# Optimization experiments

Hardware: AMD Instinct MI355X
Metric: run time of the kernel (lower is better)

## Reference

```python
import jax, jax.numpy as jnp
import numpy as np

H = 8  # num attention heads

def _ln(x, g, b, eps=1e-5):
    m = jnp.mean(x, -1, keepdims=True)
    v = jnp.mean((x - m) ** 2, -1, keepdims=True)
    return (x - m) / jnp.sqrt(v + eps) * g + b

def _mha(x, Wqkv, bqkv, Wo, bo, bias=None):
    Bn, N, D = x.shape
    d = D // H
    q = (x @ Wqkv[0].T + bqkv[0]).reshape(Bn, N, H, d)
    k = (x @ Wqkv[1].T + bqkv[1]).reshape(Bn, N, H, d)
    v = (x @ Wqkv[2].T + bqkv[2]).reshape(Bn, N, H, d)
    s = jnp.einsum('bihd,bjhd->bhij', q, k) * (1.0 / np.sqrt(d))
    if bias is not None:
        s = s + jnp.transpose(bias, (0, 3, 1, 2))  # [Bn,H,N,N] additive bias
    a = jax.nn.softmax(s, axis=-1)
    o = jnp.einsum('bhij,bjhd->bihd', a, v).reshape(Bn, N, D)
    return o @ Wo.T + bo

def _ffn(x, W1, b1, W2, b2):
    return jax.nn.relu(x @ W1.T + b1) @ W2.T + b2

def _pe(T, dim):
    pos = jnp.arange(T, dtype=jnp.float32)[:, None]
    div = jnp.exp(jnp.arange(0, dim, 2, dtype=jnp.float32) * (-np.log(10000.0) / dim))
    pe = jnp.zeros((T, dim), jnp.float32)
    pe = pe.at[:, 0::2].set(jnp.sin(pos * div))
    pe = pe.at[:, 1::2].set(jnp.cos(pos * div))
    return pe

def reference(pose, W_pose, W_emb, prelu_a, W_bias, gWqkv, gbqkv, gWo, gbo, gln1g, gln1b, gW1, gb1, gW2, gb2, gln2g, gln2b, deW, deb, tWqkv, tbqkv, tWo, tbo, tln1g, tln1b, tW1, tb1, tW2, tb2, tln2g, tln2b, W_out):
    B, C, T, V = pose.shape
    D = W_pose.shape[0]
    p = jnp.transpose(pose, (0, 2, 3, 1))  # [B,T,V,C]
    y = jnp.einsum('btvc,dc->btvd', p, W_pose).reshape(B * T, V, D)
    bias_pre = p[:, :, None, :, :] - p[:, :, :, None, :]  # [B,T,V,V,C] pairwise diffs
    pe = _pe(T, D)
    for i in range(2):
        h = jnp.einsum('btijc,hc->btijh', bias_pre, W_emb[i])  # [B,T,V,V,256]
        h = jnp.where(h >= 0, h, prelu_a[i] * h)               # PReLU
        bias = (jnp.einsum('btijh,gh->btijg', h, W_bias[i]) * (1.0 / np.sqrt(float(H)))).reshape(B * T, V, V, H)
        # GraphEncoder: post-LN transformer block with additive per-head attn bias
        a = _mha(y, gWqkv[i], gbqkv[i], gWo[i], gbo[i], bias)
        y1 = _ln(y + a, gln1g[i], gln1b[i])
        g = _ln(y1 + _ffn(y1, gW1[i], gb1[i], gW2[i], gb2[i]), gln2g[i], gln2b[i])
        g = g @ deW[i].T + deb[i]                              # gat_de linear
        # torch .view(B*V, T, -1): raw memory reinterpretation -> jnp.reshape
        y = g.reshape(B * V, T, D) + pe[None]                  # positional encoding
        mem = y
        # temporal Encoder: post-LN transformer block, no bias
        a = _mha(y, tWqkv[i], tbqkv[i], tWo[i], tbo[i])
        y1 = _ln(y + a, tln1g[i], tln1b[i])
        y = _ln(y1 + _ffn(y1, tW1[i], tb1[i], tW2[i], tb2[i]), tln2g[i], tln2b[i])
        y = (y + mem).reshape(B * T, V, D)
    out = jnp.einsum('bvd,od->bvo', y, W_out)
    out = jnp.where(out >= 0, out, 0.01 * out)  # LeakyReLU
    return out.reshape(B, -1, T, V)

def setup_inputs() -> dict:
    key = jax.random.key(0)
    ks = iter(jax.random.split(key, 64))
    def g(shape, scale):
        return jax.random.normal(next(ks), shape, jnp.float32) * scale
    B, C, T, V = 16, 32, 62, 19
    D, Hd, O = 128, 256, 64
    inp = {
        'pose': g((B, C, T, V), 1.0),
        'W_pose': g((D, C), 1.0 / np.sqrt(C)),
        'W_emb': g((2, Hd, C), 1.0 / np.sqrt(C)),
        'prelu_a': jnp.full((2,), 0.25, jnp.float32),
        'W_bias': g((2, H, Hd), 1.0 / np.sqrt(Hd)),
        'gWqkv': g((2, 3, D, D), 1.0 / np.sqrt(D)),
        'gbqkv': jnp.zeros((2, 3, D), jnp.float32),
        'gWo': g((2, D, D), 1.0 / np.sqrt(D)),
        'gbo': jnp.zeros((2, D), jnp.float32),
        'gln1g': jnp.ones((2, D), jnp.float32), 'gln1b': jnp.zeros((2, D), jnp.float32),
        'gW1': g((2, Hd, D), 1.0 / np.sqrt(D)), 'gb1': jnp.zeros((2, Hd), jnp.float32),
        'gW2': g((2, D, Hd), 1.0 / np.sqrt(Hd)), 'gb2': jnp.zeros((2, D), jnp.float32),
        'gln2g': jnp.ones((2, D), jnp.float32), 'gln2b': jnp.zeros((2, D), jnp.float32),
        'deW': g((2, D, D), 1.0 / np.sqrt(D)), 'deb': jnp.zeros((2, D), jnp.float32),
        'tWqkv': g((2, 3, D, D), 1.0 / np.sqrt(D)),
        'tbqkv': jnp.zeros((2, 3, D), jnp.float32),
        'tWo': g((2, D, D), 1.0 / np.sqrt(D)),
        'tbo': jnp.zeros((2, D), jnp.float32),
        'tln1g': jnp.ones((2, D), jnp.float32), 'tln1b': jnp.zeros((2, D), jnp.float32),
        'tW1': g((2, Hd, D), 1.0 / np.sqrt(D)), 'tb1': jnp.zeros((2, Hd), jnp.float32),
        'tW2': g((2, D, Hd), 1.0 / np.sqrt(Hd)), 'tb2': jnp.zeros((2, D), jnp.float32),
        'tln2g': jnp.ones((2, D), jnp.float32), 'tln2b': jnp.zeros((2, D), jnp.float32),
        'W_out': g((O, D), 1.0 / np.sqrt(D)),
    }
    return inp
```

## Files before the change

### kernel.cpp

```cpp
#include <hip/hip_runtime.h>
#include <hip/hip_bf16.h>
#include <math.h>

#define B_  16
#define C_  32
#define T_  62
#define V_  19
#define D_  128
#define HD_ 256
#define H_  8
#define DH_ 16
#define ROWS 18848
#define BT_ 992
#define BV_ 304

typedef __attribute__((ext_vector_type(8))) short short8v;
typedef __attribute__((ext_vector_type(4))) float f32x4;
typedef __attribute__((ext_vector_type(16))) float f32x16;

struct alignas(8) bf4 { __hip_bfloat16 x, y, z, w; };

__device__ __forceinline__ float bf2f(short s) {
    return __uint_as_float(((unsigned)(unsigned short)s) << 16);
}

__global__ void transpose_kernel(const float* __restrict__ pose, __hip_bfloat16* __restrict__ p_bf) {
    int idx = blockIdx.x * 256 + threadIdx.x;
    if (idx >= B_ * T_ * V_ * C_) return;
    int c = idx & 31;
    int rest = idx >> 5;
    int v = rest % V_;
    int rest2 = rest / V_;
    int t = rest2 % T_;
    int b = rest2 / T_;
    p_bf[idx] = __float2bfloat16(pose[((size_t)((b * C_ + c) * T_ + t)) * V_ + v]);
}

__global__ void wconv_kernel(
        const float* s0, const float* s1, const float* s2, const float* s3,
        const float* s4, const float* s5, const float* s6, const float* s7,
        const float* s8, const float* s9, const float* s10, const float* s11,
        __hip_bfloat16* __restrict__ dst) {
    int idx = blockIdx.x * 256 + threadIdx.x;
    if (idx >= 585728) return;
    const float* s; int base;
    if      (idx <   4096) { s = s0;  base = 0;      }
    else if (idx <  20480) { s = s1;  base = 4096;   }
    else if (idx < 118784) { s = s2;  base = 20480;  }
    else if (idx < 151552) { s = s3;  base = 118784; }
    else if (idx < 217088) { s = s4;  base = 151552; }
    else if (idx < 282624) { s = s5;  base = 217088; }
    else if (idx < 315392) { s = s6;  base = 282624; }
    else if (idx < 413696) { s = s7;  base = 315392; }
    else if (idx < 446464) { s = s8;  base = 413696; }
    else if (idx < 512000) { s = s9;  base = 446464; }
    else if (idx < 577536) { s = s10; base = 512000; }
    else                   { s = s11; base = 577536; }
    dst[idx] = __float2bfloat16(s[idx - base]);
}

__global__ __launch_bounds__(512) void w2_kernel(
        const float* __restrict__ Wbias, const float* __restrict__ Wemb,
        float* __restrict__ w2) {
    int tid = threadIdx.x;
    int layer = tid >> 8, g = (tid >> 5) & 7, c = tid & 31;
    float acc = 0.f;
    for (int hh = 0; hh < HD_; ++hh)
        acc += Wbias[layer * 2048 + g * HD_ + hh] * Wemb[layer * 8192 + hh * C_ + c];
    w2[layer * 256 + g * C_ + c] = acc;
}

template<int N, int K, int EPI, bool HASBIAS, bool O32, bool O16>
__global__ __launch_bounds__(256) void mfma_linear(
        const __hip_bfloat16* __restrict__ A, const __hip_bfloat16* __restrict__ W,
        const float* __restrict__ bias, float* __restrict__ out32,
        __hip_bfloat16* __restrict__ out16) {
    int wave = threadIdx.x >> 6;
    int lane = threadIdx.x & 63;
    int nt = blockIdx.y * 4 + wave;
    int n0 = nt * 32;
    if (n0 >= N) return;
    int r0 = blockIdx.x * 64;
    int r1 = r0 + 32;
    bool has2 = (r1 < ROWS);
    int rl = lane & 31;
    int kk = (lane >> 5) * 8;
    const short* Ab0 = (const short*)A + (size_t)(r0 + rl) * K + kk;
    const short* Ab1 = (const short*)A + (size_t)(r1 + rl) * K + kk;
    const short* Wb  = (const short*)W + (size_t)(n0 + rl) * K + kk;
    f32x16 acc0 = {0.f,0.f,0.f,0.f,0.f,0.f,0.f,0.f,0.f,0.f,0.f,0.f,0.f,0.f,0.f,0.f};
    f32x16 acc1 = acc0;
    #pragma unroll
    for (int kb = 0; kb < K / 16; ++kb) {
        short8v b  = *reinterpret_cast<const short8v*>(Wb  + kb * 16);
        short8v a0 = *reinterpret_cast<const short8v*>(Ab0 + kb * 16);
        acc0 = __builtin_amdgcn_mfma_f32_32x32x16_bf16(a0, b, acc0, 0, 0, 0);
        if (has2) {
            short8v a1 = *reinterpret_cast<const short8v*>(Ab1 + kb * 16);
            acc1 = __builtin_amdgcn_mfma_f32_32x32x16_bf16(a1, b, acc1, 0, 0, 0);
        }
    }
    int oc = n0 + rl;
    float bv = HASBIAS ? bias[oc] : 0.f;
    float freq = 0.f;
    if (EPI == 3) freq = expf(-(float)(oc & ~1) * (9.210340371976184f / 128.f));
    #pragma unroll
    for (int t2 = 0; t2 < 2; ++t2) {
        if (t2 == 1 && !has2) break;
        int rb = t2 ? r1 : r0;
        f32x16 acc = t2 ? acc1 : acc0;
        #pragma unroll
        for (int reg = 0; reg < 16; ++reg) {
            int orow = rb + (reg & 3) + 8 * (reg >> 2) + 4 * (lane >> 5);
            float v = acc[reg] + bv;
            if (EPI == 1) v = fmaxf(v, 0.f);
            if (EPI == 2) v = v >= 0.f ? v : 0.01f * v;
            if (EPI == 3) {
                int t = orow % T_;
                float ang = (float)t * freq;
                v += (oc & 1) ? cosf(ang) : sinf(ang);
            }
            if (O32) out32[(size_t)orow * N + oc] = v;
            if (O16) out16[(size_t)orow * N + oc] = __float2bfloat16(v);
        }
    }
}

__global__ __launch_bounds__(256) void bias2_kernel(
        const __hip_bfloat16* __restrict__ p_bf, const __hip_bfloat16* __restrict__ wemb_bf,
        const float* __restrict__ prelu_a, const float* __restrict__ Wbias,
        const float* __restrict__ w2, float* __restrict__ bias) {
    int bt = blockIdx.x;
    __shared__ float es[V_ * 257];
    __shared__ float ps[V_ * 33];
    __shared__ float f_lds[V_ * 8];
    int tid = threadIdx.x;
    if (tid < V_ * 8) {
        int v = tid >> 3, c4 = (tid & 7) * 4;
        bf4 pv = *reinterpret_cast<const bf4*>(&p_bf[((size_t)(bt * V_ + v)) * C_ + c4]);
        float* d = &ps[v * 33 + c4];
        d[0] = __bfloat162float(pv.x); d[1] = __bfloat162float(pv.y);
        d[2] = __bfloat162float(pv.z); d[3] = __bfloat162float(pv.w);
    }
    __syncthreads();
    {
        float wr[C_];
        const __hip_bfloat16* wrow = wemb_bf + (size_t)tid * C_;
        #pragma unroll
        for (int c4 = 0; c4 < 8; ++c4) {
            bf4 wv = *reinterpret_cast<const bf4*>(wrow + c4 * 4);
            wr[c4 * 4 + 0] = __bfloat162float(wv.x);
            wr[c4 * 4 + 1] = __bfloat162float(wv.y);
            wr[c4 * 4 + 2] = __bfloat162float(wv.z);
            wr[c4 * 4 + 3] = __bfloat162float(wv.w);
        }
        for (int v = 0; v < V_; ++v) {
            const float* pr = &ps[v * 33];
            float acc = 0.f;
            #pragma unroll
            for (int c = 0; c < C_; ++c) acc += pr[c] * wr[c];
            es[v * 257 + tid] = acc;
        }
    }
    if (tid < V_ * 8) {
        int v = tid >> 3, g = tid & 7;
        const float* pr = &ps[v * 33];
        const float* wr = &w2[g * C_];
        float acc = 0.f;
        #pragma unroll
        for (int c = 0; c < C_; ++c) acc += pr[c] * wr[c];
        f_lds[v * 8 + g] = acc;
    }
    __syncthreads();
    if (tid < 190) {
        int i = 0, rem = tid, cnt = V_;
        while (rem >= cnt) { rem -= cnt; ++i; --cnt; }
        int j = i + rem;
        const float a = prelu_a[0];
        const float scale = 0.35355339059327373f;
        const float cL = 0.5f * (1.f + a) * scale;
        const float cA = 0.5f * (1.f - a) * scale;
        const float* ei = es + i * 257;
        const float* ej = es + j * 257;
        float S[H_] = {0.f, 0.f, 0.f, 0.f, 0.f, 0.f, 0.f, 0.f};
        #pragma unroll 4
        for (int hh = 0; hh < HD_; ++hh) {
            float d = ej[hh] - ei[hh];
            float ad = fabsf(d);
            const float* w = Wbias + hh;
            #pragma unroll
            for (int g = 0; g < H_; ++g) S[g] += w[g * HD_] * ad;
        }
        float* bij = bias + ((size_t)bt * (V_ * V_) + i * V_ + j) * H_;
        float* bji = bias + ((size_t)bt * (V_ * V_) + j * V_ + i) * H_;
        #pragma unroll
        for (int g = 0; g < H_; ++g) {
            float lin = cL * (f_lds[j * 8 + g] - f_lds[i * 8 + g]);
            float sym = cA * S[g];
            bij[g] = lin + sym;
            bji[g] = sym - lin;
        }
    }
}

__global__ __launch_bounds__(384) void attn_graph_kernel(
        const __hip_bfloat16* __restrict__ qkv, const float* __restrict__ bias,
        __hip_bfloat16* __restrict__ out) {
    int bt = blockIdx.x;
    int h = blockIdx.y;
    __shared__ float q_lds[V_][20];
    __shared__ float k_lds[V_][20];
    __shared__ float v_lds[V_][20];
    __shared__ float sm[V_][20];
    int tid = threadIdx.x;
    for (int idx = tid; idx < V_ * 2 * 3; idx += 384) {
        int mat = idx / (V_ * 2);
        int rem = idx - mat * (V_ * 2);
        int row = rem >> 1, half = rem & 1;
        short8v v = *reinterpret_cast<const short8v*>(
            qkv + ((size_t)(bt * V_ + row)) * 384 + mat * 128 + h * DH_ + half * 8);
        float* dst = (mat == 0 ? q_lds[row] : (mat == 1 ? k_lds[row] : v_lds[row])) + half * 8;
        #pragma unroll
        for (int u = 0; u < 8; ++u) dst[u] = bf2f(v[u]);
    }
    __syncthreads();
    if (tid < V_ * V_) {
        int i = tid / V_, j = tid - i * V_;
        float acc = 0.f;
        #pragma unroll
        for (int c = 0; c < 4; ++c) {
            float4 qv = *reinterpret_cast<const float4*>(&q_lds[i][4 * c]);
            float4 kv = *reinterpret_cast<const float4*>(&k_lds[j][4 * c]);
            acc += qv.x * kv.x + qv.y * kv.y + qv.z * kv.z + qv.w * kv.w;
        }
        sm[i][j] = acc * 0.25f + bias[((size_t)(bt * V_ + i) * V_ + j) * H_ + h];
    }
    __syncthreads();
    if (tid < V_) {
        float m = -1e30f;
        for (int j = 0; j < V_; ++j) m = fmaxf(m, sm[tid][j]);
        float sum = 0.f;
        for (int j = 0; j < V_; ++j) { float e = __expf(sm[tid][j] - m); sm[tid][j] = e; sum += e; }
        float inv = 1.f / sum;
        for (int j = 0; j < V_; ++j) sm[tid][j] *= inv;
    }
    __syncthreads();
    if (tid < V_ * DH_) {
        int i = tid / DH_, d = tid - i * DH_;
        float o = 0.f;
        #pragma unroll 4
        for (int j = 0; j < V_; ++j) o += sm[i][j] * v_lds[j][d];
        out[((size_t)(bt * V_ + i)) * D_ + h * DH_ + d] = __float2bfloat16(o);
    }
}

__global__ __launch_bounds__(256) void attn_temporal_kernel(
        const __hip_bfloat16* __restrict__ qkv, __hip_bfloat16* __restrict__ out) {
    int b = blockIdx.x;
    int h = blockIdx.y;
    __shared__ float q_lds[T_][20];
    __shared__ float k_lds[T_][20];
    __shared__ float v_lds[T_][20];
    __shared__ float sm[T_][68];
    int tid = threadIdx.x;
    for (int idx = tid; idx < T_ * 2 * 3; idx += 256) {
        int mat = idx / (T_ * 2);
        int rem = idx - mat * (T_ * 2);
        int row = rem >> 1, half = rem & 1;
        short8v v = *reinterpret_cast<const short8v*>(
            qkv + ((size_t)(b * T_ + row)) * 384 + mat * 128 + h * DH_ + half * 8);
        float* dst = (mat == 0 ? q_lds[row] : (mat == 1 ? k_lds[row] : v_lds[row])) + half * 8;
        #pragma unroll
        for (int u = 0; u < 8; ++u) dst[u] = bf2f(v[u]);
    }
    __syncthreads();
    if (tid < T_ * 4) {
        int i = tid >> 2, jt = tid & 3;
        float qreg[16];
        #pragma unroll
        for (int c = 0; c < 4; ++c) {
            float4 qv = *reinterpret_cast<const float4*>(&q_lds[i][4 * c]);
            qreg[4 * c + 0] = qv.x * 0.25f;
            qreg[4 * c + 1] = qv.y * 0.25f;
            qreg[4 * c + 2] = qv.z * 0.25f;
            qreg[4 * c + 3] = qv.w * 0.25f;
        }
        float s[16];
        #pragma unroll
        for (int jj = 0; jj < 16; ++jj) {
            int j = jj * 4 + jt;
            float acc = -1e30f;
            if (j < T_) {
                acc = 0.f;
                const float* kr = k_lds[j];
                #pragma unroll
                for (int c = 0; c < 4; ++c) {
                    float4 kv = *reinterpret_cast<const float4*>(&kr[4 * c]);
                    acc += qreg[4*c+0] * kv.x + qreg[4*c+1] * kv.y
                         + qreg[4*c+2] * kv.z + qreg[4*c+3] * kv.w;
                }
            }
            s[jj] = acc;
        }
        float m = -1e30f;
        #pragma unroll
        for (int jj = 0; jj < 16; ++jj) m = fmaxf(m, s[jj]);
        m = fmaxf(m, __shfl_xor(m, 1, 64));
        m = fmaxf(m, __shfl_xor(m, 2, 64));
        float sum = 0.f;
        #pragma unroll
        for (int jj = 0; jj < 16; ++jj) {
            int j = jj * 4 + jt;
            float e = (j < T_) ? __expf(s[jj] - m) : 0.f;
            s[jj] = e;
            sum += e;
        }
        sum += __shfl_xor(sum, 1, 64);
        sum += __shfl_xor(sum, 2, 64);
        float inv = 1.f / sum;
        #pragma unroll
        for (int jj = 0; jj < 16; ++jj) {
            int j = jj * 4 + jt;
            if (j < T_) sm[i][j] = s[jj] * inv;
        }
    }
    __syncthreads();
    if (tid < T_ * 4) {
        int i = tid >> 2, dg = tid & 3;
        float4 o = {0.f, 0.f, 0.f, 0.f};
        for (int j = 0; j < T_; ++j) {
            float pp = sm[i][j];
            const float4 vv = *reinterpret_cast<const float4*>(&v_lds[j][4 * dg]);
            o.x += pp * vv.x; o.y += pp * vv.y; o.z += pp * vv.z; o.w += pp * vv.w;
        }
        bf4 ov = { __float2bfloat16(o.x), __float2bfloat16(o.y),
                   __float2bfloat16(o.z), __float2bfloat16(o.w) };
        *reinterpret_cast<bf4*>(out + ((size_t)(b * T_ + i)) * D_ + h * DH_ + 4 * dg) = ov;
    }
}

template<bool O32, bool O16>
__global__ __launch_bounds__(64) void ln_add_kernel(
        const float* __restrict__ x, const float* __restrict__ r,
        const float* __restrict__ g, const float* __restrict__ b,
        float* __restrict__ o32, __hip_bfloat16* __restrict__ o16) {
    int row = blockIdx.x;
    int lane = threadIdx.x;
    const float* xr = x + (size_t)row * D_;
    const float* rr = r + (size_t)row * D_;
    float v0 = xr[lane] + rr[lane];
    float v1 = xr[lane + 64] + rr[lane + 64];
    float s = v0 + v1, sq = v0 * v0 + v1 * v1;
    #pragma unroll
    for (int off = 32; off > 0; off >>= 1) {
        s += __shfl_xor(s, off, 64);
        sq += __shfl_xor(sq, off, 64);
    }
    float mean = s * (1.f / 128.f);
    float var = sq * (1.f / 128.f) - mean * mean;
    float rstd = rsqrtf(var + 1e-5f);
    float a0 = (v0 - mean) * rstd * g[lane]      + b[lane];
    float a1 = (v1 - mean) * rstd * g[lane + 64] + b[lane + 64];
    if (O32) {
        float* o = o32 + (size_t)row * D_;
        o[lane] = a0; o[lane + 64] = a1;
    }
    if (O16) {
        __hip_bfloat16* o = o16 + (size_t)row * D_;
        o[lane] = __float2bfloat16(a0); o[lane + 64] = __float2bfloat16(a1);
    }
}

__global__ __launch_bounds__(64) void ln_add_add_kernel(
        const float* __restrict__ x, const float* __restrict__ r,
        const float* __restrict__ g, const float* __restrict__ b,
        float* __restrict__ y, __hip_bfloat16* __restrict__ y_bf) {
    int row = blockIdx.x;
    int lane = threadIdx.x;
    const float* xr = x + (size_t)row * D_;
    const float* rr = r + (size_t)row * D_;
    float v0 = xr[lane] + rr[lane];
    float v1 = xr[lane + 64] + rr[lane + 64];
    float s = v0 + v1, sq = v0 * v0 + v1 * v1;
    #pragma unroll
    for (int off = 32; off > 0; off >>= 1) {
        s += __shfl_xor(s, off, 64);
        sq += __shfl_xor(sq, off, 64);
    }
    float mean = s * (1.f / 128.f);
    float var = sq * (1.f / 128.f) - mean * mean;
    float rstd = rsqrtf(var + 1e-5f);
    float a0 = (v0 - mean) * rstd * g[lane]      + b[lane];
    float a1 = (v1 - mean) * rstd * g[lane + 64] + b[lane + 64];
    float* yp = y + (size_t)row * D_;
    __hip_bfloat16* yb = y_bf + (size_t)row * D_;
    float y0 = yp[lane] + a0;
    float y1v = yp[lane + 64] + a1;
    yp[lane] = y0;       yb[lane] = __float2bfloat16(y0);
    yp[lane + 64] = y1v; yb[lane + 64] = __float2bfloat16(y1v);
}

extern "C" void kernel_launch(void* const* d_in, const int* in_sizes, int n_in,
                              void* d_out, int out_size, void* d_ws, size_t ws_size,
                              hipStream_t stream) {
    const float* pose    = (const float*)d_in[0];
    const float* W_pose  = (const float*)d_in[1];
    const float* W_emb   = (const float*)d_in[2];
    const float* prelu_a = (const float*)d_in[3];
    const float* W_bias  = (const float*)d_in[4];
    const float* gWqkv   = (const float*)d_in[5];
    const float* gbqkv   = (const float*)d_in[6];
    const float* gWo     = (const float*)d_in[7];
    const float* gbo     = (const float*)d_in[8];
    const float* gln1g   = (const float*)d_in[9];
    const float* gln1b   = (const float*)d_in[10];
    const float* gW1     = (const float*)d_in[11];
    const float* gb1     = (const float*)d_in[12];
    const float* gW2     = (const float*)d_in[13];
    const float* gb2     = (const float*)d_in[14];
    const float* gln2g   = (const float*)d_in[15];
    const float* gln2b   = (const float*)d_in[16];
    const float* deW     = (const float*)d_in[17];
    const float* deb     = (const float*)d_in[18];
    const float* tWqkv   = (const float*)d_in[19];
    const float* tbqkv   = (const float*)d_in[20];
    const float* tWo     = (const float*)d_in[21];
    const float* tbo     = (const float*)d_in[22];
    const float* tln1g   = (const float*)d_in[23];
    const float* tln1b   = (const float*)d_in[24];
    const float* tW1     = (const float*)d_in[25];
    const float* tb1     = (const float*)d_in[26];
    const float* tW2     = (const float*)d_in[27];
    const float* tb2     = (const float*)d_in[28];
    const float* tln2g   = (const float*)d_in[29];
    const float* tln2b   = (const float*)d_in[30];
    const float* W_out   = (const float*)d_in[31];

    float* ws = (float*)d_ws;
    __hip_bfloat16* p_bf   = (__hip_bfloat16*)(ws + 0);
    float*          y      = ws + 301568;
    __hip_bfloat16* y_bf   = (__hip_bfloat16*)(ws + 2714112);
    float*          biasbuf= ws + 3920384;
    float*          big    = ws + 6785280;
    __hip_bfloat16* qkv_bf = (__hip_bfloat16*)big;
    float*          tmp    = big;
    __hip_bfloat16* hid_bf = (__hip_bfloat16*)(big + 2412544);
    float*          y1     = big + 4825088;
    __hip_bfloat16* attn_bf= (__hip_bfloat16*)(ws + 14022912);
    float*          t2     = ws + 15229184;
    __hip_bfloat16* y1_bf  = (__hip_bfloat16*)t2;
    __hip_bfloat16* t2_bf  = (__hip_bfloat16*)t2;
    __hip_bfloat16* w_bf   = (__hip_bfloat16*)(ws + 17641728);
    float*          w2     = ws + 17934592;
    float*          outf   = (float*)d_out;

    const int oWpose = 0, oWemb = 4096, oGqkv = 20480, oGwo = 118784, oGw1 = 151552,
              oGw2 = 217088, oDe = 282624, oTqkv = 315392, oTwo = 413696,
              oTw1 = 446464, oTw2 = 512000, oWout = 577536;

    const int GX = (ROWS + 63) / 64;

    wconv_kernel<<<(585728 + 255) / 256, 256, 0, stream>>>(
        W_pose, W_emb, gWqkv, gWo, gW1, gW2, deW, tWqkv, tWo, tW1, tW2, W_out, w_bf);
    w2_kernel<<<1, 512, 0, stream>>>(W_bias, W_emb, w2);
    transpose_kernel<<<(B_*T_*V_*C_ + 255) / 256, 256, 0, stream>>>(pose, p_bf);
    mfma_linear<128, 32, 0, false, true, true><<<dim3(GX, 1), 256, 0, stream>>>(
        p_bf, w_bf + oWpose, nullptr, y, y_bf);

    for (int i = 0; i < 2; ++i) {
        bias2_kernel<<<BT_, 256, 0, stream>>>(
            p_bf, w_bf + oWemb + i * 8192, prelu_a + i,
            W_bias + (size_t)i * H_ * HD_, w2 + i * 256, biasbuf);
        mfma_linear<384, 128, 0, true, false, true><<<dim3(GX, 3), 256, 0, stream>>>(
            y_bf, w_bf + oGqkv + i * 49152, gbqkv + (size_t)i * 384, nullptr, qkv_bf);
        attn_graph_kernel<<<dim3(BT_, H_), 384, 0, stream>>>(qkv_bf, biasbuf, attn_bf);
        mfma_linear<128, 128, 0, true, true, false><<<dim3(GX, 1), 256, 0, stream>>>(
            attn_bf, w_bf + oGwo + i * 16384, gbo + (size_t)i * D_, tmp, nullptr);
        ln_add_kernel<true, true><<<ROWS, 64, 0, stream>>>(
            y, tmp, gln1g + (size_t)i * D_, gln1b + (size_t)i * D_, y1, y1_bf);
        mfma_linear<256, 128, 1, true, false, true><<<dim3(GX, 2), 256, 0, stream>>>(
            y1_bf, w_bf + oGw1 + i * 32768, gb1 + (size_t)i * HD_, nullptr, hid_bf);
        mfma_linear<128, 256, 0, true, true, false><<<dim3(GX, 1), 256, 0, stream>>>(
            hid_bf, w_bf + oGw2 + i * 32768, gb2 + (size_t)i * D_, tmp, nullptr);
        ln_add_kernel<false, true><<<ROWS, 64, 0, stream>>>(
            y1, tmp, gln2g + (size_t)i * D_, gln2b + (size_t)i * D_, nullptr, t2_bf);
        mfma_linear<128, 128, 3, true, true, true><<<dim3(GX, 1), 256, 0, stream>>>(
            t2_bf, w_bf + oDe + i * 16384, deb + (size_t)i * D_, y, y_bf);

        mfma_linear<384, 128, 0, true, false, true><<<dim3(GX, 3), 256, 0, stream>>>(
            y_bf, w_bf + oTqkv + i * 49152, tbqkv + (size_t)i * 384, nullptr, qkv_bf);
        attn_temporal_kernel<<<dim3(BV_, H_), 256, 0, stream>>>(qkv_bf, attn_bf);
        mfma_linear<128, 128, 0, true, true, false><<<dim3(GX, 1), 256, 0, stream>>>(
            attn_bf, w_bf + oTwo + i * 16384, tbo + (size_t)i * D_, tmp, nullptr);
        ln_add_kernel<true, true><<<ROWS, 64, 0, stream>>>(
            y, tmp, tln1g + (size_t)i * D_, tln1b + (size_t)i * D_, y1, y1_bf);
        mfma_linear<256, 128, 1, true, false, true><<<dim3(GX, 2), 256, 0, stream>>>(
            y1_bf, w_bf + oTw1 + i * 32768, tb1 + (size_t)i * HD_, nullptr, hid_bf);
        mfma_linear<128, 256, 0, true, true, false><<<dim3(GX, 1), 256, 0, stream>>>(
            hid_bf, w_bf + oTw2 + i * 32768, tb2 + (size_t)i * D_, tmp, nullptr);
        ln_add_add_kernel<<<ROWS, 64, 0, stream>>>(
            y1, tmp, tln2g + (size_t)i * D_, tln2b + (size_t)i * D_, y, y_bf);
    }

    mfma_linear<64, 128, 2, false, true, false><<<dim3(GX, 1), 256, 0, stream>>>(
        y_bf, w_bf + oWout, nullptr, outf, nullptr);
}
```

Measured before the change: 626.8 us.

## Fuse FFN up/down projections into one kernel with hidden kept in LDS

Adds an ffn_kernel that computes relu(x W1^T + b1) for a 32-row tile, stores the bf16 hidden activations in shared memory, then immediately applies W2 and writes the fp32 result. This removes the hidden-buffer round trip through global memory and one launch per FFN. Separately, the layernorm kernels now process four rows per 256-thread block instead of one row per 64-thread block, cutting block count. The fused kernel reloads weights from global per block with no LDS staging, and 32-row tiles may give lower MFMA reuse than the previous GEMM tiling.

```diff
diff --git a/kernel.cpp b/kernel.cpp
--- a/kernel.cpp
+++ b/kernel.cpp
@@ -126,6 +126,61 @@
     }
 }
 
+__global__ __launch_bounds__(256) void ffn_kernel(
+        const __hip_bfloat16* __restrict__ A, const __hip_bfloat16* __restrict__ W1,
+        const float* __restrict__ b1, const __hip_bfloat16* __restrict__ W2,
+        const float* __restrict__ b2, float* __restrict__ out) {
+    __shared__ __hip_bfloat16 hid[32][264];
+    int wave = threadIdx.x >> 6;
+    int lane = threadIdx.x & 63;
+    int r0 = blockIdx.x * 32;
+    int rl = lane & 31;
+    int kk = (lane >> 5) * 8;
+    const short* Ab = (const short*)A + (size_t)(r0 + rl) * D_ + kk;
+    short8v afr[8];
+    #pragma unroll
+    for (int kb = 0; kb < 8; ++kb)
+        afr[kb] = *reinterpret_cast<const short8v*>(Ab + kb * 16);
+    #pragma unroll
+    for (int pass = 0; pass < 2; ++pass) {
+        int n0 = (wave + pass * 4) * 32;
+        const short* Wb = (const short*)W1 + (size_t)(n0 + rl) * D_ + kk;
+        f32x16 acc = {0.f,0.f,0.f,0.f,0.f,0.f,0.f,0.f,0.f,0.f,0.f,0.f,0.f,0.f,0.f,0.f};
+        #pragma unroll
+        for (int kb = 0; kb < 8; ++kb) {
+            short8v b = *reinterpret_cast<const short8v*>(Wb + kb * 16);
+            acc = __builtin_amdgcn_mfma_f32_32x32x16_bf16(afr[kb], b, acc, 0, 0, 0);
+        }
+        int oc = n0 + rl;
+        float bv = b1[oc];
+        #pragma unroll
+        for (int reg = 0; reg < 16; ++reg) {
+            int orow = (reg & 3) + 8 * (reg >> 2) + 4 * (lane >> 5);
+            hid[orow][oc] = __float2bfloat16(fmaxf(acc[reg] + bv, 0.f));
+        }
+    }
+    __syncthreads();
+    {
+        int n0 = wave * 32;
+        const short* Wb = (const short*)W2 + (size_t)(n0 + rl) * HD_ + kk;
+        const short* Hrow = (const short*)&hid[rl][0];
+        f32x16 acc = {0.f,0.f,0.f,0.f,0.f,0.f,0.f,0.f,0.f,0.f,0.f,0.f,0.f,0.f,0.f,0.f};
+        #pragma unroll
+        for (int kb = 0; kb < 16; ++kb) {
+            short8v a = *reinterpret_cast<const short8v*>(Hrow + kb * 16 + kk);
+            short8v b = *reinterpret_cast<const short8v*>(Wb + kb * 16);
+            acc = __builtin_amdgcn_mfma_f32_32x32x16_bf16(a, b, acc, 0, 0, 0);
+        }
+        int oc = n0 + rl;
+        float bv = b2[oc];
+        #pragma unroll
+        for (int reg = 0; reg < 16; ++reg) {
+            int orow = r0 + (reg & 3) + 8 * (reg >> 2) + 4 * (lane >> 5);
+            out[(size_t)orow * D_ + oc] = acc[reg] + bv;
+        }
+    }
+}
+
 __global__ __launch_bounds__(256) void bias2_kernel(
         const __hip_bfloat16* __restrict__ p_bf, const __hip_bfloat16* __restrict__ wemb_bf,
         const float* __restrict__ prelu_a, const float* __restrict__ Wbias,
@@ -340,12 +395,12 @@
 }
 
 template<bool O32, bool O16>
-__global__ __launch_bounds__(64) void ln_add_kernel(
+__global__ __launch_bounds__(256) void ln_add_kernel(
         const float* __restrict__ x, const float* __restrict__ r,
         const float* __restrict__ g, const float* __restrict__ b,
         float* __restrict__ o32, __hip_bfloat16* __restrict__ o16) {
-    int row = blockIdx.x;
-    int lane = threadIdx.x;
+    int row = blockIdx.x * 4 + (threadIdx.x >> 6);
+    int lane = threadIdx.x & 63;
     const float* xr = x + (size_t)row * D_;
     const float* rr = r + (size_t)row * D_;
     float v0 = xr[lane] + rr[lane];
@@ -371,12 +426,12 @@
     }
 }
 
-__global__ __launch_bounds__(64) void ln_add_add_kernel(
+__global__ __launch_bounds__(256) void ln_add_add_kernel(
         const float* __restrict__ x, const float* __restrict__ r,
         const float* __restrict__ g, const float* __restrict__ b,
         float* __restrict__ y, __hip_bfloat16* __restrict__ y_bf) {
-    int row = blockIdx.x;
-    int lane = threadIdx.x;
+    int row = blockIdx.x * 4 + (threadIdx.x >> 6);
+    int lane = threadIdx.x & 63;
     const float* xr = x + (size_t)row * D_;
     const float* rr = r + (size_t)row * D_;
     float v0 = xr[lane] + rr[lane];
@@ -444,7 +499,6 @@
     float*          big    = ws + 6785280;
     __hip_bfloat16* qkv_bf = (__hip_bfloat16*)big;
     float*          tmp    = big;
-    __hip_bfloat16* hid_bf = (__hip_bfloat16*)(big + 2412544);
     float*          y1     = big + 4825088;
     __hip_bfloat16* attn_bf= (__hip_bfloat16*)(ws + 14022912);
     float*          t2     = ws + 15229184;
@@ -459,6 +513,7 @@
               oTw1 = 446464, oTw2 = 512000, oWout = 577536;
 
     const int GX = (ROWS + 63) / 64;
+    const int LNG = ROWS / 4;
 
     wconv_kernel<<<(585728 + 255) / 256, 256, 0, stream>>>(
         W_pose, W_emb, gWqkv, gWo, gW1, gW2, deW, tWqkv, tWo, tW1, tW2, W_out, w_bf);
@@ -476,13 +531,12 @@
         attn_graph_kernel<<<dim3(BT_, H_), 384, 0, stream>>>(qkv_bf, biasbuf, attn_bf);
         mfma_linear<128, 128, 0, true, true, false><<<dim3(GX, 1), 256, 0, stream>>>(
             attn_bf, w_bf + oGwo + i * 16384, gbo + (size_t)i * D_, tmp, nullptr);
-        ln_add_kernel<true, true><<<ROWS, 64, 0, stream>>>(
+        ln_add_kernel<true, true><<<LNG, 256, 0, stream>>>(
             y, tmp, gln1g + (size_t)i * D_, gln1b + (size_t)i * D_, y1, y1_bf);
-        mfma_linear<256, 128, 1, true, false, true><<<dim3(GX, 2), 256, 0, stream>>>(
-            y1_bf, w_bf + oGw1 + i * 32768, gb1 + (size_t)i * HD_, nullptr, hid_bf);
-        mfma_linear<128, 256, 0, true, true, false><<<dim3(GX, 1), 256, 0, stream>>>(
-            hid_bf, w_bf + oGw2 + i * 32768, gb2 + (size_t)i * D_, tmp, nullptr);
-        ln_add_kernel<false, true><<<ROWS, 64, 0, stream>>>(
+        ffn_kernel<<<ROWS / 32, 256, 0, stream>>>(
+            y1_bf, w_bf + oGw1 + i * 32768, gb1 + (size_t)i * HD_,
+            w_bf + oGw2 + i * 32768, gb2 + (size_t)i * D_, tmp);
+        ln_add_kernel<false, true><<<LNG, 256, 0, stream>>>(
             y1, tmp, gln2g + (size_t)i * D_, gln2b + (size_t)i * D_, nullptr, t2_bf);
         mfma_linear<128, 128, 3, true, true, true><<<dim3(GX, 1), 256, 0, stream>>>(
             t2_bf, w_bf + oDe + i * 16384, deb + (size_t)i * D_, y, y_bf);
@@ -492,13 +546,12 @@
         attn_temporal_kernel<<<dim3(BV_, H_), 256, 0, stream>>>(qkv_bf, attn_bf);
         mfma_linear<128, 128, 0, true, true, false><<<dim3(GX, 1), 256, 0, stream>>>(
             attn_bf, w_bf + oTwo + i * 16384, tbo + (size_t)i * D_, tmp, nullptr);
-        ln_add_kernel<true, true><<<ROWS, 64, 0, stream>>>(
+        ln_add_kernel<true, true><<<LNG, 256, 0, stream>>>(
             y, tmp, tln1g + (size_t)i * D_, tln1b + (size_t)i * D_, y1, y1_bf);
-        mfma_linear<256, 128, 1, true, false, true><<<dim3(GX, 2), 256, 0, stream>>>(
-            y1_bf, w_bf + oTw1 + i * 32768, tb1 + (size_t)i * HD_, nullptr, hid_bf);
-        mfma_linear<128, 256, 0, true, true, false><<<dim3(GX, 1), 256, 0, stream>>>(
-            hid_bf, w_bf + oTw2 + i * 32768, tb2 + (size_t)i * D_, tmp, nullptr);
-        ln_add_add_kernel<<<ROWS, 64, 0, stream>>>(
+        ffn_kernel<<<ROWS / 32, 256, 0, stream>>>(
+            y1_bf, w_bf + oTw1 + i * 32768, tb1 + (size_t)i * HD_,
+            w_bf + oTw2 + i * 32768, tb2 + (size_t)i * D_, tmp);
+        ln_add_add_kernel<<<LNG, 256, 0, stream>>>(
             y1, tmp, tln2g + (size_t)i * D_, tln2b + (size_t)i * D_, y, y_bf);
     }
 
```

New measurement: 598.9 us. 4.4% less time.
